# Performance work log

Hardware: AMD Instinct MI355X
Metric: run time of the kernel (lower is better)

Reference implementation:

```python
import jax, jax.numpy as jnp
import numpy as np

D_MODEL, D_QK, D_V = 1024, 128, 128
B, S = 4, 4096


def setup_inputs() -> dict:
    key = jax.random.key(0)
    ks = jax.random.split(key, 4)
    scale = 1.0 / np.sqrt(D_MODEL)
    return {
        "x": jax.random.normal(ks[0], (B, S, D_MODEL), dtype=jnp.float32),
        "Wq": jax.random.normal(ks[1], (D_MODEL, D_QK), dtype=jnp.float32) * scale,
        "bq": jnp.zeros((D_QK,), dtype=jnp.float32),
        "Wk": jax.random.normal(ks[2], (D_MODEL, D_QK), dtype=jnp.float32) * scale,
        "bk": jnp.zeros((D_QK,), dtype=jnp.float32),
        "Wv": jax.random.normal(ks[3], (D_MODEL, D_V), dtype=jnp.float32) * scale,
        "bv": jnp.zeros((D_V,), dtype=jnp.float32),
    }


def reference(x, Wq, bq, Wk, bk, Wv, bv):
    # Linear projections (torch Linear: x @ W^T + b; here W stored as [in, out])
    q = jnp.einsum("bsd,de->bse", x, Wq) + bq  # [B, S, d_qk]
    k = jnp.einsum("bsd,de->bse", x, Wk) + bk  # [B, S, d_qk]
    v = jnp.einsum("bsd,de->bse", x, Wv) + bv  # [B, S, d_v]
    scores = jnp.einsum("bqe,bke->bqk", q, k) / jnp.sqrt(jnp.float32(D_QK))
    attn = jax.nn.softmax(scores, axis=-1)  # [B, S, S]
    return jnp.einsum("bqk,bkv->bqv", attn, v)  # [B, S, d_v]
```

## Files before the change

### kernel.cpp

```cpp
#include <hip/hip_runtime.h>
#include <math.h>

#define DM    1024
#define DQK   128
#define BATCH 4
#define SEQ   4096
#define QSCALE (0.08838834764831845f * 1.4426950408889634f)
#define DEFER_THR 6.0f

typedef _Float16 f16;
typedef _Float16 f16x4 __attribute__((ext_vector_type(4)));
typedef _Float16 f16x8 __attribute__((ext_vector_type(8)));
typedef float    f32x4 __attribute__((ext_vector_type(4)));

__device__ __forceinline__ void stage16(const void* g, unsigned char* l) {
    __builtin_amdgcn_global_load_lds(
        (const __attribute__((address_space(1))) unsigned int*)g,
        (__attribute__((address_space(3))) unsigned int*)l, 16, 0, 0);
}

__global__ __launch_bounds__(256) void wcvt_kernel(
    const float* __restrict__ Wq, const float* __restrict__ bq,
    const float* __restrict__ Wk, const float* __restrict__ bk,
    const float* __restrict__ Wv, const float* __restrict__ bv,
    f16* __restrict__ wt, float* __restrict__ biasf)
{
    const int sel   = blockIdx.x >> 5;
    const int rem   = blockIdx.x & 31;
    const int k0    = (rem >> 2) * 128;
    const int n0    = (rem & 3) * 32;
    const float* W; const float* b; float sc;
    if (sel == 0)      { W = Wq; b = bq; sc = QSCALE; }
    else if (sel == 1) { W = Wk; b = bk; sc = 1.0f; }
    else               { W = Wv; b = bv; sc = 1.0f; }

    __shared__ f16 tile[128][40];

    #pragma unroll
    for (int it = 0; it < 16; ++it) {
        int flat = threadIdx.x + it * 256;
        int kk   = flat >> 5;
        int cc   = flat & 31;
        tile[kk][cc] = (f16)(W[(size_t)(k0 + kk) * DQK + n0 + cc] * sc);
    }
    __syncthreads();

    #pragma unroll
    for (int it = 0; it < 2; ++it) {
        int flat  = threadIdx.x + it * 256;
        int nl    = flat >> 4;
        int kc    = flat & 15;
        f16x8 v;
        #pragma unroll
        for (int i = 0; i < 8; ++i) v[i] = tile[kc * 8 + i][nl];
        *(f16x8*)(wt + (size_t)(sel * 128 + n0 + nl) * DM + k0 + kc * 8) = v;
    }
    if (rem == 0 && threadIdx.x < 128)
        biasf[sel * 128 + threadIdx.x] = b[threadIdx.x] * sc;
}

#define PXOFF 0u
#define PWOFF 16384u

__global__ __launch_bounds__(512, 2) void proj_kernel(
    const float* __restrict__ x, const f16* __restrict__ wt,
    const float* __restrict__ biasf,
    f16* __restrict__ qo, f16* __restrict__ ko, f16* __restrict__ vto)
{
    __shared__ __align__(16) unsigned char smem[114688];

    const int tid  = threadIdx.x;
    const int lane = tid & 63;
    const int w    = tid >> 6;
    const int c    = lane & 15;
    const int g    = lane >> 4;
    const int r0   = blockIdx.x * 64;

    const int srow = tid >> 3;
    const int skq  = tid & 7;
    const float* const xsrc  = x + (size_t)(r0 + srow) * DM + skq * 8;
    const unsigned     swoff = (unsigned)(srow * 128 + ((skq ^ (srow & 7)) * 16));

    const char* const wtB   = (const char*)wt;
    const unsigned    wsrcsw = (unsigned)(((lane & 7) ^ ((lane >> 3) & 7)) * 16);

    f32x4 acc[4][3];
    #pragma unroll
    for (int rf = 0; rf < 4; ++rf)
        #pragma unroll
        for (int nf = 0; nf < 3; ++nf) acc[rf][nf] = (f32x4)0.f;

    float4 xa, xb2;
    auto gload = [&](int t) {
        const float* p = xsrc + t * 64;
        xa  = *(const float4*)p;
        xb2 = *(const float4*)(p + 4);
    };
    auto swrite = [&](int buf) {
        f16x8 h;
        h[0] = (f16)xa.x;  h[1] = (f16)xa.y;  h[2] = (f16)xa.z;  h[3] = (f16)xa.w;
        h[4] = (f16)xb2.x; h[5] = (f16)xb2.y; h[6] = (f16)xb2.z; h[7] = (f16)xb2.w;
        *(f16x8*)(smem + PXOFF + (unsigned)buf * 8192u + swoff) = h;
    };
    auto stage_W = [&](int t, int pbuf) {
        unsigned char* wdst = smem + PWOFF + (unsigned)pbuf * 49152u + (unsigned)w * 1024u;
        #pragma unroll
        for (int cc = 0; cc < 6; ++cc) {
            const int j = tid + cc * 512;
            const int n = j >> 3;
            stage16(wtB + (size_t)n * 2048 + (size_t)t * 128 + wsrcsw, wdst + cc * 8192);
        }
    };

    gload(0); swrite(0);
    gload(1);
    stage_W(0, 0);
    __syncthreads();

    for (int t = 0; t < 16; ++t) {
        const int cur = t & 1;
        if (t < 15) swrite(cur ^ 1);
        if (t < 14) gload(t + 2);
        if (t < 15) stage_W(t + 1, cur ^ 1);

        f16x8 af[4][2];
        #pragma unroll
        for (int rf = 0; rf < 4; ++rf)
            #pragma unroll
            for (int ks = 0; ks < 2; ++ks)
                af[rf][ks] = *(const f16x8*)(smem + PXOFF + (unsigned)cur * 8192u
                    + (unsigned)((rf * 16 + c) * 128)
                    + (unsigned)((((4 * ks + g) ^ (c & 7)) * 16)));

        unsigned char* const wbase = smem + PWOFF + (unsigned)cur * 49152u;
        #pragma unroll
        for (int nf = 0; nf < 3; ++nf) {
            #pragma unroll
            for (int ks = 0; ks < 2; ++ks) {
                f16x8 bf = *(const f16x8*)(wbase
                    + (unsigned)((w * 48 + nf * 16 + c) * 128)
                    + (unsigned)((((4 * ks + g) ^ (c & 7)) * 16)));
                #pragma unroll
                for (int rf = 0; rf < 4; ++rf)
                    acc[rf][nf] = __builtin_amdgcn_mfma_f32_16x16x32_f16(
                        af[rf][ks], bf, acc[rf][nf], 0, 0, 0);
            }
        }
        __syncthreads();
    }

    f16* const tile = (f16*)smem;
    #pragma unroll
    for (int rf = 0; rf < 4; ++rf)
        #pragma unroll
        for (int nf = 0; nf < 3; ++nf) {
            const int n  = w * 48 + nf * 16 + c;
            const float bb = biasf[n];
            #pragma unroll
            for (int r = 0; r < 4; ++r) {
                const int row = rf * 16 + 4 * g + r;
                tile[row * 392 + n] = (f16)(acc[rf][nf][r] + bb);
            }
        }
    __syncthreads();

    #pragma unroll
    for (int it = 0; it < 2; ++it) {
        const int u   = tid + it * 512;
        const int row = u >> 4;
        const int c8  = (u & 15) * 8;
        *(f16x8*)(qo + (size_t)(r0 + row) * DQK + c8) = *(const f16x8*)&tile[row * 392 + c8];
        *(f16x8*)(ko + (size_t)(r0 + row) * DQK + c8) = *(const f16x8*)&tile[row * 392 + 128 + c8];
    }
    const int gb = r0 >> 12;
    const int s0 = r0 & (SEQ - 1);
    #pragma unroll
    for (int it = 0; it < 2; ++it) {
        const int u  = tid + it * 512;
        const int d  = u >> 3;
        const int s8 = (u & 7) * 8;
        f16x8 vv;
        #pragma unroll
        for (int i = 0; i < 8; ++i) vv[i] = tile[(s8 + i) * 392 + 256 + d];
        *(f16x8*)(vto + ((size_t)gb * DQK + d) * SEQ + s0 + s8) = vv;
    }
}

#define KOFF 0u
#define VOFF 65536u
#define POFF 131072u
#define MOFF 151552u
#define LOFF 152576u

__global__ __launch_bounds__(512, 2) void attn_kernel(
    const f16* __restrict__ qg, const f16* __restrict__ kg,
    const f16* __restrict__ vtg, float* __restrict__ out)
{
    __shared__ __align__(16) unsigned char smem[153600];

    const int tid  = threadIdx.x;
    const int lane = tid & 63;
    const int w    = tid >> 6;
    const int wq   = w >> 2;
    const int wk   = w & 3;
    const int c    = lane & 15;
    const int g    = lane >> 4;

    const int bid = blockIdx.x;
    const int xcd = bid & 7;
    const int bb  = xcd >> 1;
    const int qt  = (bid >> 3) | ((xcd & 1) << 5);
    const int q0  = qt * 64;

    const f16*  qb = qg  + (size_t)bb * SEQ * DQK;
    const char* kB = (const char*)(kg  + (size_t)bb * SEQ * DQK);
    const char* vB = (const char*)(vtg + (size_t)bb * DQK * SEQ);

    f16x8 qf[2][4];
    {
        const f16* qr = qb + (size_t)(q0 + wq * 32) * DQK;
        #pragma unroll
        for (int n = 0; n < 2; ++n)
            #pragma unroll
            for (int ks = 0; ks < 4; ++ks)
                qf[n][ks] = *(const f16x8*)(qr + (n * 16 + c) * DQK + ks * 32 + 8 * g);
    }

    f32x4 o[2][9];
    #pragma unroll
    for (int n = 0; n < 2; ++n)
        #pragma unroll
        for (int f = 0; f < 9; ++f) o[n][f] = (f32x4)0.f;
    float m_run[2] = {-3e38f, -3e38f};

    f16x8 onesf;
    #pragma unroll
    for (int i = 0; i < 8; ++i) onesf[i] = (f16)1.0f;

    const unsigned wbase = (unsigned)(tid >> 6) * 1024;

    auto stage_tiles = [&](int t, int pbuf) {
        const int kv0 = t * 128;
        unsigned char* kdst = smem + KOFF + (unsigned)pbuf * 32768u + wbase;
        unsigned char* vdst = smem + VOFF + (unsigned)pbuf * 32768u + wbase;
        #pragma unroll
        for (int cc = 0; cc < 4; ++cc) {
            const int j   = tid + cc * 512;
            const int row = j >> 4;
            const int col = j & 15;
            const int sw  = (col ^ (row & 7)) * 16;
            stage16(kB + (size_t)(kv0 + row) * 256 + sw, kdst + cc * 8192);
            stage16(vB + (size_t)row * 8192 + (size_t)kv0 * 2 + sw, vdst + cc * 8192);
        }
    };

    stage_tiles(0, 0);
    __syncthreads();

    unsigned char* const pmine = smem + POFF + (unsigned)w * 2560u;

    for (int t = 0; t < 32; ++t) {
        const int pb = t & 1;
        if (t < 31) stage_tiles(t + 1, pb ^ 1);

        unsigned char* const kbase = smem + KOFF + (unsigned)pb * 32768u;
        unsigned char* const vbase = smem + VOFF + (unsigned)pb * 32768u;

        f32x4 s[2][2];
        s[0][0] = (f32x4)0.f; s[0][1] = (f32x4)0.f;
        s[1][0] = (f32x4)0.f; s[1][1] = (f32x4)0.f;
        __builtin_amdgcn_s_setprio(1);
        #pragma unroll
        for (int ks = 0; ks < 4; ++ks) {
            #pragma unroll
            for (int m = 0; m < 2; ++m) {
                f16x8 kf = *(const f16x8*)(kbase
                    + (unsigned)(wk * 32 + m * 16 + c) * 256u
                    + (unsigned)(((4 * ks + g) ^ (c & 7)) * 16));
                s[m][0] = __builtin_amdgcn_mfma_f32_16x16x32_f16(kf, qf[0][ks], s[m][0], 0, 0, 0);
                s[m][1] = __builtin_amdgcn_mfma_f32_16x16x32_f16(kf, qf[1][ks], s[m][1], 0, 0, 0);
            }
        }
        __builtin_amdgcn_s_setprio(0);

        float mt[2];
        #pragma unroll
        for (int n = 0; n < 2; ++n) {
            float a0 = fmaxf(fmaxf(s[0][n][0], s[0][n][1]), fmaxf(s[0][n][2], s[0][n][3]));
            float a1 = fmaxf(fmaxf(s[1][n][0], s[1][n][1]), fmaxf(s[1][n][2], s[1][n][3]));
            float v  = fmaxf(a0, a1);
            v = fmaxf(v, __shfl_xor(v, 16, 64));
            v = fmaxf(v, __shfl_xor(v, 32, 64));
            mt[n] = v;
        }

        bool need = (mt[0] > m_run[0] + DEFER_THR) || (mt[1] > m_run[1] + DEFER_THR);
        if (__any(need)) {
            float al[2];
            #pragma unroll
            for (int n = 0; n < 2; ++n) {
                float mn = fmaxf(m_run[n], mt[n]);
                al[n] = __builtin_amdgcn_exp2f(m_run[n] - mn);
                m_run[n] = mn;
            }
            float alo[2][4];
            #pragma unroll
            for (int n = 0; n < 2; ++n)
                #pragma unroll
                for (int r = 0; r < 4; ++r)
                    alo[n][r] = __shfl(al[n], 4 * g + r, 16);
            #pragma unroll
            for (int n = 0; n < 2; ++n)
                #pragma unroll
                for (int f = 0; f < 9; ++f)
                    #pragma unroll
                    for (int r = 0; r < 4; ++r) o[n][f][r] *= alo[n][r];
        }

        #pragma unroll
        for (int n = 0; n < 2; ++n)
            #pragma unroll
            for (int m = 0; m < 2; ++m) {
                f16x4 h;
                #pragma unroll
                for (int r = 0; r < 4; ++r)
                    h[r] = (f16)__builtin_amdgcn_exp2f(s[m][n][r] - m_run[n]);
                *(f16x4*)(pmine + (unsigned)(16 * n + c) * 80u + (unsigned)(32 * m + 8 * g)) = h;
            }

        f16x8 pa[2];
        pa[0] = *(const f16x8*)(pmine + (unsigned)(c) * 80u + 16u * g);
        pa[1] = *(const f16x8*)(pmine + (unsigned)(16 + c) * 80u + 16u * g);
        __builtin_amdgcn_s_setprio(1);
        #pragma unroll
        for (int df = 0; df < 8; ++df) {
            f16x8 vf = *(const f16x8*)(vbase
                + (unsigned)(df * 16 + c) * 256u
                + (unsigned)(((4 * wk + g) ^ (c & 7)) * 16));
            o[0][df] = __builtin_amdgcn_mfma_f32_16x16x32_f16(pa[0], vf, o[0][df], 0, 0, 0);
            o[1][df] = __builtin_amdgcn_mfma_f32_16x16x32_f16(pa[1], vf, o[1][df], 0, 0, 0);
        }
        o[0][8] = __builtin_amdgcn_mfma_f32_16x16x32_f16(pa[0], onesf, o[0][8], 0, 0, 0);
        o[1][8] = __builtin_amdgcn_mfma_f32_16x16x32_f16(pa[1], onesf, o[1][8], 0, 0, 0);
        __builtin_amdgcn_s_setprio(0);

        __syncthreads();
    }

    float m_o[2][4];
    #pragma unroll
    for (int n = 0; n < 2; ++n)
        #pragma unroll
        for (int r = 0; r < 4; ++r)
            m_o[n][r] = __shfl(m_run[n], 4 * g + r, 16);

    float* const mld  = (float*)(smem + MOFF);
    float* const lld  = (float*)(smem + LOFF);
    float* const olds = (float*)smem;

    if (wk > 0) {
        const int base = (wq * 3 + (wk - 1)) * 32;
        #pragma unroll
        for (int n = 0; n < 2; ++n)
            #pragma unroll
            for (int f = 0; f < 8; ++f)
                #pragma unroll
                for (int r = 0; r < 4; ++r)
                    olds[(size_t)(base + n * 16 + 4 * g + r) * 132 + f * 16 + c] = o[n][f][r];
        if (c == 0) {
            #pragma unroll
            for (int n = 0; n < 2; ++n)
                #pragma unroll
                for (int r = 0; r < 4; ++r) {
                    mld[(wq * 4 + wk) * 32 + n * 16 + 4 * g + r] = m_o[n][r];
                    lld[(wq * 4 + wk) * 32 + n * 16 + 4 * g + r] = o[n][8][r];
                }
        }
    }
    __syncthreads();

    if (wk == 0) {
        #pragma unroll
        for (int n = 0; n < 2; ++n) {
            #pragma unroll
            for (int r = 0; r < 4; ++r) {
                const int rl = n * 16 + 4 * g + r;
                const float m0 = m_o[n][r];
                const float m1 = mld[(wq * 4 + 1) * 32 + rl];
                const float m2 = mld[(wq * 4 + 2) * 32 + rl];
                const float m3 = mld[(wq * 4 + 3) * 32 + rl];
                const float ms = fmaxf(fmaxf(m0, m1), fmaxf(m2, m3));
                const float a0 = __builtin_amdgcn_exp2f(m0 - ms);
                const float a1 = __builtin_amdgcn_exp2f(m1 - ms);
                const float a2 = __builtin_amdgcn_exp2f(m2 - ms);
                const float a3 = __builtin_amdgcn_exp2f(m3 - ms);
                const float ls = a0 * o[n][8][r]
                               + a1 * lld[(wq * 4 + 1) * 32 + rl]
                               + a2 * lld[(wq * 4 + 2) * 32 + rl]
                               + a3 * lld[(wq * 4 + 3) * 32 + rl];
                const float inv = 1.0f / ls;
                float* orow = out + ((size_t)bb * SEQ + q0 + wq * 32 + rl) * DQK;
                #pragma unroll
                for (int f = 0; f < 8; ++f) {
                    float v = a0 * o[n][f][r]
                            + a1 * olds[(size_t)((wq * 3 + 0) * 32 + rl) * 132 + f * 16 + c]
                            + a2 * olds[(size_t)((wq * 3 + 1) * 32 + rl) * 132 + f * 16 + c]
                            + a3 * olds[(size_t)((wq * 3 + 2) * 32 + rl) * 132 + f * 16 + c];
                    orow[f * 16 + c] = v * inv;
                }
            }
        }
    }
}

extern "C" void kernel_launch(void* const* d_in, const int* in_sizes, int n_in,
                              void* d_out, int out_size, void* d_ws, size_t ws_size,
                              hipStream_t stream) {
    const float* x  = (const float*)d_in[0];
    const float* Wq = (const float*)d_in[1];
    const float* bq = (const float*)d_in[2];
    const float* Wk = (const float*)d_in[3];
    const float* bk = (const float*)d_in[4];
    const float* Wv = (const float*)d_in[5];
    const float* bv = (const float*)d_in[6];
    float* outp = (float*)d_out;

    f16*   qf    = (f16*)d_ws;
    f16*   kf    = qf + (size_t)BATCH * SEQ * DQK;
    f16*   vt    = kf + (size_t)BATCH * SEQ * DQK;
    f16*   wt    = vt + (size_t)BATCH * DQK * SEQ;
    float* biasf = (float*)(wt + (size_t)384 * DM);

    wcvt_kernel<<<96, 256, 0, stream>>>(Wq, bq, Wk, bk, Wv, bv, wt, biasf);

    proj_kernel<<<BATCH * SEQ / 64, 512, 0, stream>>>(x, wt, biasf, qf, kf, vt);

    attn_kernel<<<256, 512, 0, stream>>>(qf, kf, vt, outp);
}
```

Measured before the change: 90.86 us.

## Load projection weights directly into registers in MFMA-fragment layout, drop LDS staging

The weight-conversion kernel now writes the transposed fp16 weights in a layout that matches the MFMA B-fragment order. The projection kernel then loads each wave's weight fragments straight from global memory into registers, double-buffered, instead of staging them through LDS. This cuts LDS use from about 112KB to about 49KB, and the launch bound rises to allow 4 blocks per CU. In exchange, each block rereads the weights from global or L2 memory without sharing them, and the extra buffer registers must fit the tighter register budget.

After: 89.70 us. About the same (-1.3%).

```diff
diff --git a/kernel.cpp b/kernel.cpp
--- a/kernel.cpp
+++ b/kernel.cpp
@@ -53,21 +53,23 @@
         f16x8 v;
         #pragma unroll
         for (int i = 0; i < 8; ++i) v[i] = tile[kc * 8 + i][nl];
-        *(f16x8*)(wt + (size_t)(sel * 128 + n0 + nl) * DM + k0 + kc * 8) = v;
+        const int N  = sel * 128 + n0 + nl;
+        const int NF = N >> 4;
+        const int c2 = N & 15;
+        const int KS = (k0 >> 5) + (kc >> 2);
+        const int gg = kc & 3;
+        *(f16x8*)(wt + (size_t)(NF * 32 + KS) * 512 + c2 * 32 + gg * 8) = v;
     }
     if (rem == 0 && threadIdx.x < 128)
         biasf[sel * 128 + threadIdx.x] = b[threadIdx.x] * sc;
 }
 
-#define PXOFF 0u
-#define PWOFF 16384u
-
-__global__ __launch_bounds__(512, 2) void proj_kernel(
-    const float* __restrict__ x, const f16* __restrict__ wt,
+__global__ __launch_bounds__(512, 4) void proj_kernel(
+    const float* __restrict__ x, const f16* __restrict__ wt2,
     const float* __restrict__ biasf,
     f16* __restrict__ qo, f16* __restrict__ ko, f16* __restrict__ vto)
 {
-    __shared__ __align__(16) unsigned char smem[114688];
+    __shared__ __align__(16) unsigned char smem[50176];
 
     const int tid  = threadIdx.x;
     const int lane = tid & 63;
@@ -81,8 +83,7 @@
     const float* const xsrc  = x + (size_t)(r0 + srow) * DM + skq * 8;
     const unsigned     swoff = (unsigned)(srow * 128 + ((skq ^ (srow & 7)) * 16));
 
-    const char* const wtB   = (const char*)wt;
-    const unsigned    wsrcsw = (unsigned)(((lane & 7) ^ ((lane >> 3) & 7)) * 16);
+    const f16* const wl = wt2 + (size_t)(w * 3) * 32 * 512 + c * 32 + g * 8;
 
     f32x4 acc[4][3];
     #pragma unroll
@@ -100,51 +101,53 @@
         f16x8 h;
         h[0] = (f16)xa.x;  h[1] = (f16)xa.y;  h[2] = (f16)xa.z;  h[3] = (f16)xa.w;
         h[4] = (f16)xb2.x; h[5] = (f16)xb2.y; h[6] = (f16)xb2.z; h[7] = (f16)xb2.w;
-        *(f16x8*)(smem + PXOFF + (unsigned)buf * 8192u + swoff) = h;
+        *(f16x8*)(smem + (unsigned)buf * 8192u + swoff) = h;
     };
-    auto stage_W = [&](int t, int pbuf) {
-        unsigned char* wdst = smem + PWOFF + (unsigned)pbuf * 49152u + (unsigned)w * 1024u;
-        #pragma unroll
-        for (int cc = 0; cc < 6; ++cc) {
-            const int j = tid + cc * 512;
-            const int n = j >> 3;
-            stage16(wtB + (size_t)n * 2048 + (size_t)t * 128 + wsrcsw, wdst + cc * 8192);
-        }
-    };
+
+    f16x8 bC[6], bN[6];
 
     gload(0); swrite(0);
     gload(1);
-    stage_W(0, 0);
+    #pragma unroll
+    for (int nf = 0; nf < 3; ++nf)
+        #pragma unroll
+        for (int ks = 0; ks < 2; ++ks)
+            bC[nf * 2 + ks] = *(const f16x8*)(wl + nf * 16384 + ks * 512);
     __syncthreads();
 
     for (int t = 0; t < 16; ++t) {
         const int cur = t & 1;
         if (t < 15) swrite(cur ^ 1);
         if (t < 14) gload(t + 2);
-        if (t < 15) stage_W(t + 1, cur ^ 1);
-
-        f16x8 af[4][2];
-        #pragma unroll
-        for (int rf = 0; rf < 4; ++rf)
-            #pragma unroll
-            for (int ks = 0; ks < 2; ++ks)
-                af[rf][ks] = *(const f16x8*)(smem + PXOFF + (unsigned)cur * 8192u
-                    + (unsigned)((rf * 16 + c) * 128)
-                    + (unsigned)((((4 * ks + g) ^ (c & 7)) * 16)));
-
-        unsigned char* const wbase = smem + PWOFF + (unsigned)cur * 49152u;
-        #pragma unroll
-        for (int nf = 0; nf < 3; ++nf) {
-            #pragma unroll
-            for (int ks = 0; ks < 2; ++ks) {
-                f16x8 bf = *(const f16x8*)(wbase
-                    + (unsigned)((w * 48 + nf * 16 + c) * 128)
-                    + (unsigned)((((4 * ks + g) ^ (c & 7)) * 16)));
-                #pragma unroll
-                for (int rf = 0; rf < 4; ++rf)
-                    acc[rf][nf] = __builtin_amdgcn_mfma_f32_16x16x32_f16(
-                        af[rf][ks], bf, acc[rf][nf], 0, 0, 0);
-            }
+        if (t < 15) {
+            #pragma unroll
+            for (int nf = 0; nf < 3; ++nf)
+                #pragma unroll
+                for (int ks = 0; ks < 2; ++ks)
+                    bN[nf * 2 + ks] = *(const f16x8*)(wl + nf * 16384
+                                                      + ((t + 1) * 2 + ks) * 512);
+        }
+
+        #pragma unroll
+        for (int rf = 0; rf < 4; ++rf) {
+            f16x8 af0 = *(const f16x8*)(smem + (unsigned)cur * 8192u
+                + (unsigned)((rf * 16 + c) * 128)
+                + (unsigned)(((g) ^ (c & 7)) * 16));
+            f16x8 af1 = *(const f16x8*)(smem + (unsigned)cur * 8192u
+                + (unsigned)((rf * 16 + c) * 128)
+                + (unsigned)((((4 + g) ^ (c & 7)) * 16)));
+            #pragma unroll
+            for (int nf = 0; nf < 3; ++nf) {
+                acc[rf][nf] = __builtin_amdgcn_mfma_f32_16x16x32_f16(
+                    af0, bC[nf * 2 + 0], acc[rf][nf], 0, 0, 0);
+                acc[rf][nf] = __builtin_amdgcn_mfma_f32_16x16x32_f16(
+                    af1, bC[nf * 2 + 1], acc[rf][nf], 0, 0, 0);
+            }
+        }
+
+        if (t < 15) {
+            #pragma unroll
+            for (int j = 0; j < 6; ++j) bC[j] = bN[j];
         }
         __syncthreads();
     }
```
